# Kernel tuning notes

Hardware: AMD Instinct MI355X
Metric: run time of the kernel (lower is better)

The kernel has to match this reference:

```python
import jax, jax.numpy as jnp
import numpy as np

N_NODES = 50000   # field_size == number of graph nodes
N_EDGES = 800000  # avg degree 16
VOCAB = 200000    # feature_size
EMB = 64          # embedding_size == in_dim
HID = 64          # num_hidden
SLOPE = 0.2       # leaky relu negative slope


def setup_inputs() -> dict:
    key = jax.random.key(0)
    ks = jax.random.split(key, 20)
    s = 0.05
    d = {}
    d["features"] = jax.random.randint(ks[0], (8, N_NODES), 0, VOCAB, dtype=jnp.int32)
    d["feature_values"] = jax.random.uniform(ks[1], (8, N_NODES), dtype=jnp.float32)
    d["src"] = jax.random.randint(ks[2], (N_EDGES,), 0, N_NODES, dtype=jnp.int32)
    d["dst"] = jax.random.randint(ks[3], (N_EDGES,), 0, N_NODES, dtype=jnp.int32)
    d["emb"] = jax.random.normal(ks[4], (VOCAB, EMB), jnp.float32) * s
    # layer 0: in=64 -> heads=2, out=64 (no residual)
    d["W0"]  = jax.random.normal(ks[5], (EMB, 2 * HID), jnp.float32) * s
    d["al0"] = jax.random.normal(ks[6], (2, HID), jnp.float32) * s
    d["ar0"] = jax.random.normal(ks[7], (2, HID), jnp.float32) * s
    d["b0"]  = jnp.zeros((2 * HID,), jnp.float32)
    # layer 1: in=128 -> heads=2, out=64 (identity residual since in == heads*out)
    d["W1"]  = jax.random.normal(ks[8], (2 * HID, 2 * HID), jnp.float32) * s
    d["al1"] = jax.random.normal(ks[9], (2, HID), jnp.float32) * s
    d["ar1"] = jax.random.normal(ks[10], (2, HID), jnp.float32) * s
    d["b1"]  = jnp.zeros((2 * HID,), jnp.float32)
    # output layer: in=128 -> heads=1, out=64 (projected residual), no activation
    d["W2"]    = jax.random.normal(ks[11], (2 * HID, EMB), jnp.float32) * s
    d["al2"]   = jax.random.normal(ks[12], (1, EMB), jnp.float32) * s
    d["ar2"]   = jax.random.normal(ks[13], (1, EMB), jnp.float32) * s
    d["b2"]    = jnp.zeros((EMB,), jnp.float32)
    d["resW2"] = jax.random.normal(ks[14], (2 * HID, EMB), jnp.float32) * s
    return d


def _gat_layer(h, src, dst, W, al, ar, b, res, act):
    """DGL-style GATConv. h: [N, in], W: [in, H*D], al/ar: [H, D]."""
    N = h.shape[0]
    H, D = al.shape
    fh = (h @ W).reshape(N, H, D)                      # [N, H, D]
    el = jnp.einsum('nhd,hd->nh', fh, al)              # [N, H]
    er = jnp.einsum('nhd,hd->nh', fh, ar)              # [N, H]
    e = jax.nn.leaky_relu(el[src] + er[dst], SLOPE)    # [E, H]
    # edge softmax grouped by destination node
    m = jax.ops.segment_max(e, dst, num_segments=N)
    m = jnp.where(jnp.isfinite(m), m, 0.0)
    ex = jnp.exp(e - m[dst])
    den = jax.ops.segment_sum(ex, dst, num_segments=N)
    alpha = ex / jnp.maximum(den[dst], 1e-9)           # [E, H]
    out = jax.ops.segment_sum(alpha[:, :, None] * fh[src], dst, num_segments=N)  # [N, H, D]
    if res is not None:
        out = out + res
    out = out + b.reshape(H, D)
    if act:
        out = jax.nn.elu(out)
    return out


def reference(features, feature_values, src, dst, emb,
              W0, al0, ar0, b0, W1, al1, ar1, b1,
              W2, al2, ar2, b2, resW2):
    # embedding lookup scaled by feature values: [B, field, emb]
    fe = emb[features] * feature_values[..., None]
    h = fe[0]                                          # [N_NODES, EMB]
    # layer 0: no residual, elu, flatten heads
    h = _gat_layer(h, src, dst, W0, al0, ar0, b0, None, True).reshape(N_NODES, -1)
    # layer 1: identity residual (in == heads*out), elu, flatten heads
    res1 = h.reshape(N_NODES, 2, HID)
    h = _gat_layer(h, src, dst, W1, al1, ar1, b1, res1, True).reshape(N_NODES, -1)
    # output layer: projected residual, no activation, mean over heads
    res2 = (h @ resW2).reshape(N_NODES, 1, EMB)
    logits = _gat_layer(h, src, dst, W2, al2, ar2, b2, res2, False).mean(axis=1)
    return logits
```

## Files before the change

kernel.cpp:

```cpp
#include <hip/hip_runtime.h>


typedef __attribute__((ext_vector_type(8))) short short8;
typedef __attribute__((ext_vector_type(4))) float float4v;

__device__ __forceinline__ float lrelu(float x){ return x >= 0.f ? x : 0.2f*x; }

__device__ __forceinline__ unsigned short f2bf(float f){
  unsigned int u = __float_as_uint(f);
  u += 0x7fffu + ((u >> 16) & 1u);
  return (unsigned short)(u >> 16);
}
__device__ __forceinline__ float bf2f(unsigned short u){
  return __uint_as_float((unsigned int)u << 16);
}
__device__ __forceinline__ float rl_f(float v, int l){
  return __int_as_float(__builtin_amdgcn_readlane(__float_as_int(v), l));
}

__global__ void k_zero_i32(int* __restrict__ p, int n){
  int i = blockIdx.x*blockDim.x + threadIdx.x;
  if (i < n) p[i] = 0;
}

__global__ void k_hist(const int* __restrict__ dst, int* __restrict__ counts, int E){
  int i0 = (blockIdx.x*blockDim.x + threadIdx.x)*4;
  #pragma unroll
  for (int u = 0; u < 4; u++){
    int i = i0 + u;
    if (i < E) atomicAdd(&counts[dst[i]], 1);
  }
}

__global__ void k_scan_local(const int* __restrict__ counts, int* __restrict__ row_ptr,
                             int* __restrict__ bsum, int N){
  __shared__ int s[256];
  int t = threadIdx.x, g = blockIdx.x*256 + t;
  int v = (g < N) ? counts[g] : 0;
  s[t] = v; __syncthreads();
  #pragma unroll
  for (int off = 1; off < 256; off <<= 1){
    int x = 0;
    if (t >= off) x = s[t-off];
    __syncthreads();
    s[t] += x;
    __syncthreads();
  }
  if (g < N) row_ptr[g+1] = s[t];
  if (g == 0 && t == 0) row_ptr[0] = 0;
  if (t == 255) bsum[blockIdx.x] = s[255];
}

__global__ void k_scan_top(int* __restrict__ bsum, int nb){
  __shared__ int s[256];
  int t = threadIdx.x;
  int v = (t < nb) ? bsum[t] : 0;
  s[t] = v; __syncthreads();
  #pragma unroll
  for (int off = 1; off < 256; off <<= 1){
    int x = 0;
    if (t >= off) x = s[t-off];
    __syncthreads();
    s[t] += x;
    __syncthreads();
  }
  if (t < nb) bsum[t] = s[t] - v;
}

__global__ void k_scan_fix(int* __restrict__ row_ptr, const int* __restrict__ bsum, int N){
  int g = blockIdx.x*256 + threadIdx.x;
  if (g < N && blockIdx.x > 0) row_ptr[g+1] += bsum[blockIdx.x];
}

__global__ void k_scatter(const int* __restrict__ src, const int* __restrict__ dst,
                          const int* __restrict__ row_ptr, int* __restrict__ cursor,
                          unsigned short* __restrict__ ssrc, int E){
  int i0 = (blockIdx.x*blockDim.x + threadIdx.x)*4;
  #pragma unroll
  for (int u = 0; u < 4; u++){
    int i = i0 + u;
    if (i < E){
      int d = dst[i];
      int pos = atomicAdd(&cursor[d], 1);
      ssrc[row_ptr[d] + pos] = (unsigned short)src[i];
    }
  }
}

__global__ void k_wprep_all(const float* __restrict__ W0, const float* __restrict__ W1,
                            const float* __restrict__ W2, const float* __restrict__ rW2,
                            unsigned short* __restrict__ Wt0, unsigned short* __restrict__ Wt1,
                            unsigned short* __restrict__ Wt2){
  int id = blockIdx.x*256 + threadIdx.x;
  if (id < 128*64){
    int n = id/64, k = id%64;
    Wt0[n*64 + k] = f2bf(W0[k*128 + n]);
  } else if (id < 128*64 + 128*128){
    int j = id - 128*64; int n = j/128, k = j%128;
    Wt1[n*128 + k] = f2bf(W1[k*128 + n]);
  } else if (id < 128*64 + 2*128*128){
    int j = id - 128*64 - 128*128; int n = j/128, k = j%128;
    float v = (n < 64) ? W2[k*64 + n] : rW2[k*64 + (n - 64)];
    Wt2[n*128 + k] = f2bf(v);
  }
}

template<int IN, int H, int AMODE>
__global__ __launch_bounds__(256) void k_gemm_mfma(
    const float* __restrict__ hf,
    const int* __restrict__ feat, const float* __restrict__ fv, const float* __restrict__ emb,
    const unsigned short* __restrict__ Wt,
    const float* __restrict__ al, const float* __restrict__ ar,
    unsigned short* __restrict__ fhb,
    float* __restrict__ elr, int N){
  constexpr int KS = IN/32;
  constexpr int LDP = IN + 8;
  __shared__ unsigned short Wt_s[128*LDP];
  const int t = threadIdx.x;
  const int lane = t & 63, wid = t >> 6;
  const int l15 = lane & 15, quad = lane >> 4;
  const int row0 = blockIdx.x*64 + wid*16;

  for (int id = t; id < 128*(IN/8); id += 256){
    int r = id/(IN/8), seg = id%(IN/8);
    ((uint4*)(Wt_s + r*LDP))[seg] = ((const uint4*)(Wt + (size_t)r*IN))[seg];
  }
  short8 a[KS];
  int arow = row0 + l15;
  {
    const float* ap = nullptr;
    float sc = 1.f;
    if (AMODE == 0){
      int f = 0; sc = 0.f;
      if (arow < N){ f = feat[arow]; sc = fv[arow]; }
      ap = emb + (size_t)f*64;
    } else {
      ap = (arow < N) ? hf + (size_t)arow*IN : nullptr;
    }
    #pragma unroll
    for (int s = 0; s < KS; s++){
      short8 av = short8{0,0,0,0,0,0,0,0};
      if (ap){
        const float* p = ap + s*32 + quad*8;
        float4 v0 = ((const float4*)p)[0];
        float4 v1 = ((const float4*)p)[1];
        av[0]=(short)f2bf(v0.x*sc); av[1]=(short)f2bf(v0.y*sc);
        av[2]=(short)f2bf(v0.z*sc); av[3]=(short)f2bf(v0.w*sc);
        av[4]=(short)f2bf(v1.x*sc); av[5]=(short)f2bf(v1.y*sc);
        av[6]=(short)f2bf(v1.z*sc); av[7]=(short)f2bf(v1.w*sc);
      }
      a[s] = av;
    }
  }
  __syncthreads();

  float4v acc[8];
  #pragma unroll
  for (int nt = 0; nt < 8; nt++) acc[nt] = float4v{0.f,0.f,0.f,0.f};
  #pragma unroll
  for (int nt = 0; nt < 8; nt++){
    #pragma unroll
    for (int s = 0; s < KS; s++){
      short8 b = *(const short8*)(Wt_s + (nt*16 + l15)*LDP + s*32 + quad*8);
      acc[nt] = __builtin_amdgcn_mfma_f32_16x16x32_bf16(a[s], b, acc[nt], 0, 0, 0);
    }
  }

  float alc[8], arc[8];
  #pragma unroll
  for (int nt = 0; nt < 8; nt++){
    bool hv = (H == 2) || (nt < 4);
    alc[nt] = hv ? al[nt*16 + l15] : 0.f;
    arc[nt] = hv ? ar[nt*16 + l15] : 0.f;
  }
  #pragma unroll
  for (int reg = 0; reg < 4; reg++){
    int row = row0 + quad*4 + reg;
    bool rv = row < N;
    if (rv){
      #pragma unroll
      for (int nt = 0; nt < 8; nt++)
        fhb[(size_t)row*128 + nt*16 + l15] = f2bf(acc[nt][reg]);
    }
    float pel0 = 0.f, per0 = 0.f, pel1 = 0.f, per1 = 0.f;
    #pragma unroll
    for (int nt = 0; nt < 4; nt++){
      pel0 += acc[nt][reg]*alc[nt];     per0 += acc[nt][reg]*arc[nt];
      pel1 += acc[nt+4][reg]*alc[nt+4]; per1 += acc[nt+4][reg]*arc[nt+4];
    }
    #pragma unroll
    for (int off = 1; off < 16; off <<= 1){
      pel0 += __shfl_xor(pel0, off, 64);
      pel1 += __shfl_xor(pel1, off, 64);
      per0 += __shfl_xor(per0, off, 64);
      per1 += __shfl_xor(per1, off, 64);
    }
    if (l15 == 0 && rv){
      elr[row*4+0] = pel0;
      elr[row*4+1] = (H == 2) ? pel1 : 0.f;
      elr[row*4+2] = per0;
      elr[row*4+3] = (H == 2) ? per1 : 0.f;
    }
  }
}

template<int H>
__global__ __launch_bounds__(256) void k_agg(
    const unsigned* __restrict__ fhb, const float* __restrict__ elr,
    const int* __restrict__ row_ptr, const unsigned short* __restrict__ ssrc,
    const float* __restrict__ bias, const float* __restrict__ res,
    int act, int res_from_fh,
    float* __restrict__ out, int out_ld, int N){
  int lane = threadIdx.x & 63, wid = threadIdx.x >> 6;
  int n = blockIdx.x*4 + wid;
  if (n >= N) return;
  int beg = row_ptr[n], end = row_ptr[n+1];
  float er0 = elr[n*4+2];
  float er1 = (H == 2) ? elr[n*4+3] : 0.f;

  float x0 = 0.f, x1 = 0.f;
  {
    int i = beg + lane;
    if (i < end){
      int s = ssrc[i];
      float2 el = *(const float2*)(elr + s*4);
      x0 = __expf(fminf(lrelu(el.x + er0), 30.f));
      if (H == 2) x1 = __expf(fminf(lrelu(el.y + er1), 30.f));
    }
  }
  float d0 = x0, d1 = x1;
  for (int i = beg + lane + 64; i < end; i += 64){
    int s = ssrc[i];
    float2 el = *(const float2*)(elr + s*4);
    d0 += __expf(fminf(lrelu(el.x + er0), 30.f));
    if (H == 2) d1 += __expf(fminf(lrelu(el.y + er1), 30.f));
  }
  #pragma unroll
  for (int off = 32; off >= 1; off >>= 1){
    d0 += __shfl_xor(d0, off, 64);
    if (H == 2) d1 += __shfl_xor(d1, off, 64);
  }
  float rd0 = d0 > 0.f ? 1.f/d0 : 0.f;
  float rd1 = (H == 2 && d1 > 0.f) ? 1.f/d1 : 0.f;

  float ax = 0.f, ay = 0.f;
  for (int base = beg; base < end; base += 64){
    int i = base + lane;
    int s = 0; float a0 = 0.f, a1 = 0.f;
    if (i < end){
      s = ssrc[i];
      if (base == beg){
        a0 = x0 * rd0; if (H == 2) a1 = x1 * rd1;
      } else {
        float2 el = *(const float2*)(elr + s*4);
        a0 = __expf(fminf(lrelu(el.x + er0), 30.f)) * rd0;
        if (H == 2) a1 = __expf(fminf(lrelu(el.y + er1), 30.f)) * rd1;
      }
    }
    int cnt = min(64, end - base);
    int j0 = 0;
    if (H == 2){
      for (; j0 + 16 <= cnt; j0 += 16){
        unsigned w[16]; float aj[16];
        #pragma unroll
        for (int u = 0; u < 16; u++){
          int sj = __builtin_amdgcn_readlane(s, j0 + u);
          w[u] = fhb[(size_t)sj*64 + lane];
        }
        #pragma unroll
        for (int u = 0; u < 16; u++){
          float aj0 = rl_f(a0, j0 + u);
          float aj1 = rl_f(a1, j0 + u);
          aj[u] = (lane < 32) ? aj0 : aj1;
        }
        #pragma unroll
        for (int u = 0; u < 16; u++){
          ax += bf2f((unsigned short)(w[u] & 0xffffu)) * aj[u];
          ay += bf2f((unsigned short)(w[u] >> 16))     * aj[u];
        }
      }
      for (; j0 < cnt; j0 += 8){
        unsigned w[8]; float aj[8];
        #pragma unroll
        for (int u = 0; u < 8; u++){
          int sj = __builtin_amdgcn_readlane(s, j0 + u);
          w[u] = fhb[(size_t)sj*64 + lane];
        }
        #pragma unroll
        for (int u = 0; u < 8; u++){
          float aj0 = rl_f(a0, j0 + u);
          float aj1 = rl_f(a1, j0 + u);
          aj[u] = (lane < 32) ? aj0 : aj1;
        }
        #pragma unroll
        for (int u = 0; u < 8; u++){
          ax += bf2f((unsigned short)(w[u] & 0xffffu)) * aj[u];
          ay += bf2f((unsigned short)(w[u] >> 16))     * aj[u];
        }
      }
    } else {
      const unsigned short* fh16 = (const unsigned short*)fhb;
      for (; j0 + 16 <= cnt; j0 += 16){
        unsigned short w[16]; float aj[16];
        #pragma unroll
        for (int u = 0; u < 16; u++){
          int sj = __builtin_amdgcn_readlane(s, j0 + u);
          w[u] = fh16[(size_t)sj*128 + lane];
        }
        #pragma unroll
        for (int u = 0; u < 16; u++) aj[u] = rl_f(a0, j0 + u);
        #pragma unroll
        for (int u = 0; u < 16; u++) ax += bf2f(w[u]) * aj[u];
      }
      for (; j0 < cnt; j0 += 8){
        unsigned short w[8]; float aj[8];
        #pragma unroll
        for (int u = 0; u < 8; u++){
          int sj = __builtin_amdgcn_readlane(s, j0 + u);
          w[u] = fh16[(size_t)sj*128 + lane];
        }
        #pragma unroll
        for (int u = 0; u < 8; u++) aj[u] = rl_f(a0, j0 + u);
        #pragma unroll
        for (int u = 0; u < 8; u++) ax += bf2f(w[u]) * aj[u];
      }
    }
  }
  if (H == 2){
    int c0 = lane*2;
    float o0 = ax + bias[c0], o1 = ay + bias[c0+1];
    if (res){ o0 += res[n*128 + c0]; o1 += res[n*128 + c0+1]; }
    if (act){ o0 = o0 > 0.f ? o0 : expm1f(o0); o1 = o1 > 0.f ? o1 : expm1f(o1); }
    *(float2*)(out + n*out_ld + c0) = make_float2(o0, o1);
  } else {
    const unsigned short* fh16 = (const unsigned short*)fhb;
    float o = ax + bias[lane];
    if (res_from_fh) o += bf2f(fh16[(size_t)n*128 + 64 + lane]);
    out[n*out_ld + lane] = o;
  }
}

extern "C" void kernel_launch(void* const* d_in, const int* in_sizes, int n_in,
                              void* d_out, int out_size, void* d_ws, size_t ws_size,
                              hipStream_t stream) {
  const int*   feat = (const int*)  d_in[0];
  const float* fv   = (const float*)d_in[1];
  const int*   src  = (const int*)  d_in[2];
  const int*   dst  = (const int*)  d_in[3];
  const float* emb  = (const float*)d_in[4];
  const float* W0   = (const float*)d_in[5];
  const float* al0  = (const float*)d_in[6];
  const float* ar0  = (const float*)d_in[7];
  const float* b0   = (const float*)d_in[8];
  const float* W1   = (const float*)d_in[9];
  const float* al1  = (const float*)d_in[10];
  const float* ar1  = (const float*)d_in[11];
  const float* b1   = (const float*)d_in[12];
  const float* W2   = (const float*)d_in[13];
  const float* al2  = (const float*)d_in[14];
  const float* ar2  = (const float*)d_in[15];
  const float* b2   = (const float*)d_in[16];
  const float* rW2  = (const float*)d_in[17];
  const int N = in_sizes[0] / 8;
  const int E = in_sizes[2];

  size_t off = 0;
  auto alloc = [&](size_t bytes) -> void* {
    void* p = (char*)d_ws + off;
    off = (off + bytes + 255) & ~(size_t)255;
    return p;
  };
  unsigned short* P1 = (unsigned short*)alloc((size_t)N*128*sizeof(unsigned short));
  float* P2     = (float*)alloc((size_t)N*128*sizeof(float));
  float* P3     = (float*)alloc((size_t)N*128*sizeof(float));
  float* elr    = (float*)alloc((size_t)N*4*sizeof(float));
  int* row_ptr  = (int*)alloc((size_t)(N+1)*sizeof(int));
  int* counts   = (int*)alloc((size_t)2*N*sizeof(int));
  int* cursor   = counts + N;
  unsigned short* ssrc = (unsigned short*)alloc((size_t)E*sizeof(unsigned short));
  int* bsum     = (int*)alloc(256*sizeof(int));
  unsigned short* Wt0 = (unsigned short*)alloc((size_t)128*64*sizeof(unsigned short));
  unsigned short* Wt1 = (unsigned short*)alloc((size_t)128*128*sizeof(unsigned short));
  unsigned short* Wt2 = (unsigned short*)alloc((size_t)128*128*sizeof(unsigned short));

  int nb1 = (N + 255) / 256;
  k_zero_i32<<<(2*N + 255)/256, 256, 0, stream>>>(counts, 2*N);
  k_hist<<<(E/4 + 255)/256, 256, 0, stream>>>(dst, counts, E);
  k_scan_local<<<nb1, 256, 0, stream>>>(counts, row_ptr, bsum, N);
  k_scan_top<<<1, 256, 0, stream>>>(bsum, nb1);
  k_scan_fix<<<nb1, 256, 0, stream>>>(row_ptr, bsum, N);
  k_scatter<<<(E/4 + 255)/256, 256, 0, stream>>>(src, dst, row_ptr, cursor, ssrc, E);
  k_wprep_all<<<(128*64 + 2*128*128 + 255)/256, 256, 0, stream>>>(
      W0, W1, W2, rW2, Wt0, Wt1, Wt2);

  int gt = (N + 63)/64;
  int nagg = (N + 3)/4;
  k_gemm_mfma<64,2,0><<<gt, 256, 0, stream>>>(nullptr, feat, fv, emb,
      Wt0, al0, ar0, P1, elr, N);
  k_agg<2><<<nagg, 256, 0, stream>>>((unsigned*)P1, elr, row_ptr, ssrc, b0, nullptr,
                                     1, 0, P2, 128, N);
  k_gemm_mfma<128,2,1><<<gt, 256, 0, stream>>>(P2, nullptr, nullptr, nullptr,
      Wt1, al1, ar1, P1, elr, N);
  k_agg<2><<<nagg, 256, 0, stream>>>((unsigned*)P1, elr, row_ptr, ssrc, b1, P2,
                                     1, 0, P3, 128, N);
  k_gemm_mfma<128,1,1><<<gt, 256, 0, stream>>>(P3, nullptr, nullptr, nullptr,
      Wt2, al2, ar2, P1, elr, N);
  k_agg<1><<<nagg, 256, 0, stream>>>((unsigned*)P1, elr, row_ptr, ssrc, b2, nullptr,
                                     0, 1, (float*)d_out, 64, N);
}
```

Before: 374.3 us.

## Split wavefront into two half-waves gathering two neighbor rows with wider loads

The aggregation kernel now has each half of the 64-lane wavefront process a different neighbor. Each lane loads 8 bytes (uint2) of the bf16 feature row instead of 4, or 4 bytes instead of 2 in the single-head case, and accumulates four partial sums. A final cross-half shuffle combines the halves, and only 32 lanes write wider float4/float2 outputs. The aim is to halve the number of serialized gather instructions per neighbor and widen memory transactions, at the cost of an extra shuffle reduction and idle lanes in the epilogue. The zero-fill kernel is also replaced by hipMemsetAsync.

```diff
diff --git a/kernel.cpp b/kernel.cpp
--- a/kernel.cpp
+++ b/kernel.cpp
@@ -16,11 +16,6 @@
 }
 __device__ __forceinline__ float rl_f(float v, int l){
   return __int_as_float(__builtin_amdgcn_readlane(__float_as_int(v), l));
-}
-
-__global__ void k_zero_i32(int* __restrict__ p, int n){
-  int i = blockIdx.x*blockDim.x + threadIdx.x;
-  if (i < n) p[i] = 0;
 }
 
 __global__ void k_hist(const int* __restrict__ dst, int* __restrict__ counts, int E){
@@ -243,7 +238,11 @@
   float rd0 = d0 > 0.f ? 1.f/d0 : 0.f;
   float rd1 = (H == 2 && d1 > 0.f) ? 1.f/d1 : 0.f;
 
-  float ax = 0.f, ay = 0.f;
+  const int hl = lane & 31;
+  const bool loA = lane < 32;
+  const bool hi16 = (lane & 16) != 0;
+
+  float ac0 = 0.f, ac1 = 0.f, ac2 = 0.f, ac3 = 0.f;
   for (int base = beg; base < end; base += 64){
     int i = base + lane;
     int s = 0; float a0 = 0.f, a1 = 0.f;
@@ -261,82 +260,126 @@
     int j0 = 0;
     if (H == 2){
       for (; j0 + 16 <= cnt; j0 += 16){
-        unsigned w[16]; float aj[16];
-        #pragma unroll
-        for (int u = 0; u < 16; u++){
-          int sj = __builtin_amdgcn_readlane(s, j0 + u);
-          w[u] = fhb[(size_t)sj*64 + lane];
-        }
-        #pragma unroll
-        for (int u = 0; u < 16; u++){
-          float aj0 = rl_f(a0, j0 + u);
-          float aj1 = rl_f(a1, j0 + u);
-          aj[u] = (lane < 32) ? aj0 : aj1;
-        }
-        #pragma unroll
-        for (int u = 0; u < 16; u++){
-          ax += bf2f((unsigned short)(w[u] & 0xffffu)) * aj[u];
-          ay += bf2f((unsigned short)(w[u] >> 16))     * aj[u];
+        uint2 w[8]; float aj[8];
+        #pragma unroll
+        for (int p = 0; p < 8; p++){
+          int sA = __builtin_amdgcn_readlane(s, j0 + 2*p);
+          int sB = __builtin_amdgcn_readlane(s, j0 + 2*p + 1);
+          int r = loA ? sA : sB;
+          w[p] = *(const uint2*)(fhb + (size_t)r*64 + hl*2);
+        }
+        #pragma unroll
+        for (int p = 0; p < 8; p++){
+          float a0A = rl_f(a0, j0 + 2*p),   a1A = rl_f(a1, j0 + 2*p);
+          float a0B = rl_f(a0, j0 + 2*p+1), a1B = rl_f(a1, j0 + 2*p+1);
+          float a0s = loA ? a0A : a0B, a1s = loA ? a1A : a1B;
+          aj[p] = hi16 ? a1s : a0s;
+        }
+        #pragma unroll
+        for (int p = 0; p < 8; p++){
+          ac0 += bf2f((unsigned short)(w[p].x & 0xffffu)) * aj[p];
+          ac1 += bf2f((unsigned short)(w[p].x >> 16))     * aj[p];
+          ac2 += bf2f((unsigned short)(w[p].y & 0xffffu)) * aj[p];
+          ac3 += bf2f((unsigned short)(w[p].y >> 16))     * aj[p];
         }
       }
       for (; j0 < cnt; j0 += 8){
+        uint2 w[4]; float aj[4];
+        #pragma unroll
+        for (int p = 0; p < 4; p++){
+          int sA = __builtin_amdgcn_readlane(s, j0 + 2*p);
+          int sB = __builtin_amdgcn_readlane(s, j0 + 2*p + 1);
+          int r = loA ? sA : sB;
+          w[p] = *(const uint2*)(fhb + (size_t)r*64 + hl*2);
+        }
+        #pragma unroll
+        for (int p = 0; p < 4; p++){
+          float a0A = rl_f(a0, j0 + 2*p),   a1A = rl_f(a1, j0 + 2*p);
+          float a0B = rl_f(a0, j0 + 2*p+1), a1B = rl_f(a1, j0 + 2*p+1);
+          float a0s = loA ? a0A : a0B, a1s = loA ? a1A : a1B;
+          aj[p] = hi16 ? a1s : a0s;
+        }
+        #pragma unroll
+        for (int p = 0; p < 4; p++){
+          ac0 += bf2f((unsigned short)(w[p].x & 0xffffu)) * aj[p];
+          ac1 += bf2f((unsigned short)(w[p].x >> 16))     * aj[p];
+          ac2 += bf2f((unsigned short)(w[p].y & 0xffffu)) * aj[p];
+          ac3 += bf2f((unsigned short)(w[p].y >> 16))     * aj[p];
+        }
+      }
+    } else {
+      for (; j0 + 16 <= cnt; j0 += 16){
         unsigned w[8]; float aj[8];
         #pragma unroll
-        for (int u = 0; u < 8; u++){
-          int sj = __builtin_amdgcn_readlane(s, j0 + u);
-          w[u] = fhb[(size_t)sj*64 + lane];
-        }
-        #pragma unroll
-        for (int u = 0; u < 8; u++){
-          float aj0 = rl_f(a0, j0 + u);
-          float aj1 = rl_f(a1, j0 + u);
-          aj[u] = (lane < 32) ? aj0 : aj1;
-        }
-        #pragma unroll
-        for (int u = 0; u < 8; u++){
-          ax += bf2f((unsigned short)(w[u] & 0xffffu)) * aj[u];
-          ay += bf2f((unsigned short)(w[u] >> 16))     * aj[u];
-        }
-      }
-    } else {
-      const unsigned short* fh16 = (const unsigned short*)fhb;
-      for (; j0 + 16 <= cnt; j0 += 16){
-        unsigned short w[16]; float aj[16];
-        #pragma unroll
-        for (int u = 0; u < 16; u++){
-          int sj = __builtin_amdgcn_readlane(s, j0 + u);
-          w[u] = fh16[(size_t)sj*128 + lane];
-        }
-        #pragma unroll
-        for (int u = 0; u < 16; u++) aj[u] = rl_f(a0, j0 + u);
-        #pragma unroll
-        for (int u = 0; u < 16; u++) ax += bf2f(w[u]) * aj[u];
+        for (int p = 0; p < 8; p++){
+          int sA = __builtin_amdgcn_readlane(s, j0 + 2*p);
+          int sB = __builtin_amdgcn_readlane(s, j0 + 2*p + 1);
+          int r = loA ? sA : sB;
+          w[p] = fhb[(size_t)r*64 + hl];
+        }
+        #pragma unroll
+        for (int p = 0; p < 8; p++){
+          float aA = rl_f(a0, j0 + 2*p), aB = rl_f(a0, j0 + 2*p+1);
+          aj[p] = loA ? aA : aB;
+        }
+        #pragma unroll
+        for (int p = 0; p < 8; p++){
+          ac0 += bf2f((unsigned short)(w[p] & 0xffffu)) * aj[p];
+          ac1 += bf2f((unsigned short)(w[p] >> 16))     * aj[p];
+        }
       }
       for (; j0 < cnt; j0 += 8){
-        unsigned short w[8]; float aj[8];
-        #pragma unroll
-        for (int u = 0; u < 8; u++){
-          int sj = __builtin_amdgcn_readlane(s, j0 + u);
-          w[u] = fh16[(size_t)sj*128 + lane];
-        }
-        #pragma unroll
-        for (int u = 0; u < 8; u++) aj[u] = rl_f(a0, j0 + u);
-        #pragma unroll
-        for (int u = 0; u < 8; u++) ax += bf2f(w[u]) * aj[u];
-      }
-    }
-  }
+        unsigned w[4]; float aj[4];
+        #pragma unroll
+        for (int p = 0; p < 4; p++){
+          int sA = __builtin_amdgcn_readlane(s, j0 + 2*p);
+          int sB = __builtin_amdgcn_readlane(s, j0 + 2*p + 1);
+          int r = loA ? sA : sB;
+          w[p] = fhb[(size_t)r*64 + hl];
+        }
+        #pragma unroll
+        for (int p = 0; p < 4; p++){
+          float aA = rl_f(a0, j0 + 2*p), aB = rl_f(a0, j0 + 2*p+1);
+          aj[p] = loA ? aA : aB;
+        }
+        #pragma unroll
+        for (int p = 0; p < 4; p++){
+          ac0 += bf2f((unsigned short)(w[p] & 0xffffu)) * aj[p];
+          ac1 += bf2f((unsigned short)(w[p] >> 16))     * aj[p];
+        }
+      }
+    }
+  }
+  ac0 += __shfl_xor(ac0, 32, 64);
+  ac1 += __shfl_xor(ac1, 32, 64);
+  if (H == 2){ ac2 += __shfl_xor(ac2, 32, 64); ac3 += __shfl_xor(ac3, 32, 64); }
+
   if (H == 2){
-    int c0 = lane*2;
-    float o0 = ax + bias[c0], o1 = ay + bias[c0+1];
-    if (res){ o0 += res[n*128 + c0]; o1 += res[n*128 + c0+1]; }
-    if (act){ o0 = o0 > 0.f ? o0 : expm1f(o0); o1 = o1 > 0.f ? o1 : expm1f(o1); }
-    *(float2*)(out + n*out_ld + c0) = make_float2(o0, o1);
+    if (lane < 32){
+      int c0 = hl*4;
+      float4 b4 = *(const float4*)(bias + c0);
+      float o0 = ac0 + b4.x, o1 = ac1 + b4.y, o2 = ac2 + b4.z, o3 = ac3 + b4.w;
+      if (res){
+        float4 r4 = *(const float4*)(res + (size_t)n*128 + c0);
+        o0 += r4.x; o1 += r4.y; o2 += r4.z; o3 += r4.w;
+      }
+      if (act){
+        o0 = o0 > 0.f ? o0 : expm1f(o0); o1 = o1 > 0.f ? o1 : expm1f(o1);
+        o2 = o2 > 0.f ? o2 : expm1f(o2); o3 = o3 > 0.f ? o3 : expm1f(o3);
+      }
+      *(float4*)(out + (size_t)n*out_ld + c0) = make_float4(o0, o1, o2, o3);
+    }
   } else {
-    const unsigned short* fh16 = (const unsigned short*)fhb;
-    float o = ax + bias[lane];
-    if (res_from_fh) o += bf2f(fh16[(size_t)n*128 + 64 + lane]);
-    out[n*out_ld + lane] = o;
+    if (lane < 32){
+      int c0 = hl*2;
+      float o0 = ac0 + bias[c0], o1 = ac1 + bias[c0+1];
+      if (res_from_fh){
+        unsigned rw = fhb[(size_t)n*64 + 32 + hl];
+        o0 += bf2f((unsigned short)(rw & 0xffffu));
+        o1 += bf2f((unsigned short)(rw >> 16));
+      }
+      *(float2*)(out + (size_t)n*out_ld + c0) = make_float2(o0, o1);
+    }
   }
 }
 
@@ -384,7 +427,7 @@
   unsigned short* Wt2 = (unsigned short*)alloc((size_t)128*128*sizeof(unsigned short));
 
   int nb1 = (N + 255) / 256;
-  k_zero_i32<<<(2*N + 255)/256, 256, 0, stream>>>(counts, 2*N);
+  hipMemsetAsync(counts, 0, (size_t)2*N*sizeof(int), stream);
   k_hist<<<(E/4 + 255)/256, 256, 0, stream>>>(dst, counts, E);
   k_scan_local<<<nb1, 256, 0, stream>>>(counts, row_ptr, bsum, N);
   k_scan_top<<<1, 256, 0, stream>>>(bsum, nb1);
```

After: 382.5 us. 2.2% more time.

## Fuse all stages into one persistent cooperative kernel with grid syncs

Applied to the files above, without the earlier changes.

Replaces the twelve separate launches (CSR build, weight prep, three GEMM plus aggregation layer pairs) with one cooperative persistent kernel. Phases are separated by grid.sync and use grid-stride loops, and the old multi-launch path is kept as a fallback. The goal is to remove per-launch overhead and tail gaps between small kernels. The fused GEMM phase reads weights straight from global memory instead of staging them in LDS. Each grid-wide barrier costs time, and the grid is capped at 4 blocks per CU, which may limit latency hiding in the gather-bound aggregation.

```diff
diff --git a/kernel.cpp b/kernel.cpp
--- a/kernel.cpp
+++ b/kernel.cpp
@@ -1,5 +1,8 @@
 #include <hip/hip_runtime.h>
-
+#include <hip/hip_cooperative_groups.h>
+
+
+namespace cg = cooperative_groups;
 
 typedef __attribute__((ext_vector_type(8))) short short8;
 typedef __attribute__((ext_vector_type(4))) float float4v;
@@ -18,326 +21,407 @@
   return __int_as_float(__builtin_amdgcn_readlane(__float_as_int(v), l));
 }
 
-__global__ void k_zero_i32(int* __restrict__ p, int n){
-  int i = blockIdx.x*blockDim.x + threadIdx.x;
-  if (i < n) p[i] = 0;
-}
-
-__global__ void k_hist(const int* __restrict__ dst, int* __restrict__ counts, int E){
-  int i0 = (blockIdx.x*blockDim.x + threadIdx.x)*4;
+
+__device__ void wprep_body(const float* W0, const float* W1, const float* W2,
+                           const float* rW2, unsigned short* Wt0,
+                           unsigned short* Wt1, unsigned short* Wt2,
+                           int gtid, int gsz){
+  for (int id = gtid; id < 128*64 + 2*128*128; id += gsz){
+    if (id < 128*64){
+      int n = id/64, k = id%64;
+      Wt0[n*64 + k] = f2bf(W0[k*128 + n]);
+    } else if (id < 128*64 + 128*128){
+      int j = id - 128*64; int n = j/128, k = j%128;
+      Wt1[n*128 + k] = f2bf(W1[k*128 + n]);
+    } else {
+      int j = id - 128*64 - 128*128; int n = j/128, k = j%128;
+      float v = (n < 64) ? W2[k*64 + n] : rW2[k*64 + (n - 64)];
+      Wt2[n*128 + k] = f2bf(v);
+    }
+  }
+}
+
+__device__ void hist_body(const int* dst, int* counts, int E, int gtid, int gsz){
+  for (int base = gtid*4; base < E; base += gsz*4){
+    #pragma unroll
+    for (int u = 0; u < 4; u++){
+      int i = base + u;
+      if (i < E) atomicAdd(&counts[dst[i]], 1);
+    }
+  }
+}
+
+__device__ void scatter_body(const int* src, const int* dst, const int* row_ptr,
+                             int* cursor, unsigned short* ssrc, int E,
+                             int gtid, int gsz){
+  for (int base = gtid*4; base < E; base += gsz*4){
+    #pragma unroll
+    for (int u = 0; u < 4; u++){
+      int i = base + u;
+      if (i < E){
+        int d = dst[i];
+        int pos = atomicAdd(&cursor[d], 1);
+        ssrc[row_ptr[d] + pos] = (unsigned short)src[i];
+      }
+    }
+  }
+}
+
+template<int IN, int H, int AMODE>
+__device__ void gemm_phase(
+    const float* __restrict__ hf,
+    const int* __restrict__ feat, const float* __restrict__ fv, const float* __restrict__ emb,
+    const unsigned short* __restrict__ Wt,
+    const float* __restrict__ al, const float* __restrict__ ar,
+    unsigned short* __restrict__ fhb, float* __restrict__ elr,
+    int N, int bid, int nb, int t){
+  constexpr int KS = IN/32;
+  const int lane = t & 63, wid = t >> 6;
+  const int l15 = lane & 15, quad = lane >> 4;
+
+  float alc[8], arc[8];
   #pragma unroll
-  for (int u = 0; u < 4; u++){
-    int i = i0 + u;
-    if (i < E) atomicAdd(&counts[dst[i]], 1);
-  }
-}
-
-__global__ void k_scan_local(const int* __restrict__ counts, int* __restrict__ row_ptr,
-                             int* __restrict__ bsum, int N){
+  for (int nt = 0; nt < 8; nt++){
+    bool hv = (H == 2) || (nt < 4);
+    alc[nt] = hv ? al[nt*16 + l15] : 0.f;
+    arc[nt] = hv ? ar[nt*16 + l15] : 0.f;
+  }
+
+  const int ntiles = (N + 63)/64;
+  for (int tile = bid; tile < ntiles; tile += nb){
+    const int row0 = tile*64 + wid*16;
+    short8 a[KS];
+    int arow = row0 + l15;
+    {
+      const float* ap = nullptr;
+      float sc = 1.f;
+      if (AMODE == 0){
+        int f = 0; sc = 0.f;
+        if (arow < N){ f = feat[arow]; sc = fv[arow]; }
+        ap = emb + (size_t)f*64;
+      } else {
+        ap = (arow < N) ? hf + (size_t)arow*IN : nullptr;
+      }
+      #pragma unroll
+      for (int s = 0; s < KS; s++){
+        short8 av = short8{0,0,0,0,0,0,0,0};
+        if (ap){
+          const float* p = ap + s*32 + quad*8;
+          float4 v0 = ((const float4*)p)[0];
+          float4 v1 = ((const float4*)p)[1];
+          av[0]=(short)f2bf(v0.x*sc); av[1]=(short)f2bf(v0.y*sc);
+          av[2]=(short)f2bf(v0.z*sc); av[3]=(short)f2bf(v0.w*sc);
+          av[4]=(short)f2bf(v1.x*sc); av[5]=(short)f2bf(v1.y*sc);
+          av[6]=(short)f2bf(v1.z*sc); av[7]=(short)f2bf(v1.w*sc);
+        }
+        a[s] = av;
+      }
+    }
+    float4v acc[8];
+    #pragma unroll
+    for (int nt = 0; nt < 8; nt++) acc[nt] = float4v{0.f,0.f,0.f,0.f};
+    #pragma unroll
+    for (int nt = 0; nt < 8; nt++){
+      #pragma unroll
+      for (int s = 0; s < KS; s++){
+        short8 b = *(const short8*)(Wt + (size_t)(nt*16 + l15)*IN + s*32 + quad*8);
+        acc[nt] = __builtin_amdgcn_mfma_f32_16x16x32_bf16(a[s], b, acc[nt], 0, 0, 0);
+      }
+    }
+    #pragma unroll
+    for (int reg = 0; reg < 4; reg++){
+      int row = row0 + quad*4 + reg;
+      bool rv = row < N;
+      if (rv){
+        #pragma unroll
+        for (int nt = 0; nt < 8; nt++)
+          fhb[(size_t)row*128 + nt*16 + l15] = f2bf(acc[nt][reg]);
+      }
+      float pel0 = 0.f, per0 = 0.f, pel1 = 0.f, per1 = 0.f;
+      #pragma unroll
+      for (int nt = 0; nt < 4; nt++){
+        pel0 += acc[nt][reg]*alc[nt];     per0 += acc[nt][reg]*arc[nt];
+        pel1 += acc[nt+4][reg]*alc[nt+4]; per1 += acc[nt+4][reg]*arc[nt+4];
+      }
+      #pragma unroll
+      for (int off = 1; off < 16; off <<= 1){
+        pel0 += __shfl_xor(pel0, off, 64);
+        pel1 += __shfl_xor(pel1, off, 64);
+        per0 += __shfl_xor(per0, off, 64);
+        per1 += __shfl_xor(per1, off, 64);
+      }
+      if (l15 == 0 && rv){
+        elr[row*4+0] = pel0;
+        elr[row*4+1] = (H == 2) ? pel1 : 0.f;
+        elr[row*4+2] = per0;
+        elr[row*4+3] = (H == 2) ? per1 : 0.f;
+      }
+    }
+  }
+}
+
+template<int H>
+__device__ void agg_phase(
+    const unsigned* __restrict__ fhb, const float* __restrict__ elr,
+    const int* __restrict__ row_ptr, const unsigned short* __restrict__ ssrc,
+    const float* __restrict__ bias, const float* __restrict__ res,
+    int act, int res_from_fh,
+    float* __restrict__ out, int out_ld, int N, int bid, int nb, int t){
+  const int lane = t & 63, wid = t >> 6;
+  for (int n = bid*4 + wid; n < N; n += nb*4){
+    int beg = row_ptr[n], end = row_ptr[n+1];
+    float er0 = elr[n*4+2];
+    float er1 = (H == 2) ? elr[n*4+3] : 0.f;
+
+    float x0 = 0.f, x1 = 0.f;
+    {
+      int i = beg + lane;
+      if (i < end){
+        int s = ssrc[i];
+        float2 el = *(const float2*)(elr + s*4);
+        x0 = __expf(fminf(lrelu(el.x + er0), 30.f));
+        if (H == 2) x1 = __expf(fminf(lrelu(el.y + er1), 30.f));
+      }
+    }
+    float d0 = x0, d1 = x1;
+    for (int i = beg + lane + 64; i < end; i += 64){
+      int s = ssrc[i];
+      float2 el = *(const float2*)(elr + s*4);
+      d0 += __expf(fminf(lrelu(el.x + er0), 30.f));
+      if (H == 2) d1 += __expf(fminf(lrelu(el.y + er1), 30.f));
+    }
+    #pragma unroll
+    for (int off = 32; off >= 1; off >>= 1){
+      d0 += __shfl_xor(d0, off, 64);
+      if (H == 2) d1 += __shfl_xor(d1, off, 64);
+    }
+    float rd0 = d0 > 0.f ? 1.f/d0 : 0.f;
+    float rd1 = (H == 2 && d1 > 0.f) ? 1.f/d1 : 0.f;
+
+    float ax = 0.f, ay = 0.f;
+    for (int base = beg; base < end; base += 64){
+      int i = base + lane;
+      int s = 0; float a0 = 0.f, a1 = 0.f;
+      if (i < end){
+        s = ssrc[i];
+        if (base == beg){
+          a0 = x0 * rd0; if (H == 2) a1 = x1 * rd1;
+        } else {
+          float2 el = *(const float2*)(elr + s*4);
+          a0 = __expf(fminf(lrelu(el.x + er0), 30.f)) * rd0;
+          if (H == 2) a1 = __expf(fminf(lrelu(el.y + er1), 30.f)) * rd1;
+        }
+      }
+      int cnt = min(64, end - base);
+      int j0 = 0;
+      if (H == 2){
+        for (; j0 + 16 <= cnt; j0 += 16){
+          unsigned w[16]; float aj[16];
+          #pragma unroll
+          for (int u = 0; u < 16; u++){
+            int sj = __builtin_amdgcn_readlane(s, j0 + u);
+            w[u] = fhb[(size_t)sj*64 + lane];
+          }
+          #pragma unroll
+          for (int u = 0; u < 16; u++){
+            float aj0 = rl_f(a0, j0 + u);
+            float aj1 = rl_f(a1, j0 + u);
+            aj[u] = (lane < 32) ? aj0 : aj1;
+          }
+          #pragma unroll
+          for (int u = 0; u < 16; u++){
+            ax += bf2f((unsigned short)(w[u] & 0xffffu)) * aj[u];
+            ay += bf2f((unsigned short)(w[u] >> 16))     * aj[u];
+          }
+        }
+        for (; j0 < cnt; j0 += 8){
+          unsigned w[8]; float aj[8];
+          #pragma unroll
+          for (int u = 0; u < 8; u++){
+            int sj = __builtin_amdgcn_readlane(s, j0 + u);
+            w[u] = fhb[(size_t)sj*64 + lane];
+          }
+          #pragma unroll
+          for (int u = 0; u < 8; u++){
+            float aj0 = rl_f(a0, j0 + u);
+            float aj1 = rl_f(a1, j0 + u);
+            aj[u] = (lane < 32) ? aj0 : aj1;
+          }
+          #pragma unroll
+          for (int u = 0; u < 8; u++){
+            ax += bf2f((unsigned short)(w[u] & 0xffffu)) * aj[u];
+            ay += bf2f((unsigned short)(w[u] >> 16))     * aj[u];
+          }
+        }
+      } else {
+        const unsigned short* fh16 = (const unsigned short*)fhb;
+        for (; j0 + 16 <= cnt; j0 += 16){
+          unsigned short w[16]; float aj[16];
+          #pragma unroll
+          for (int u = 0; u < 16; u++){
+            int sj = __builtin_amdgcn_readlane(s, j0 + u);
+            w[u] = fh16[(size_t)sj*128 + lane];
+          }
+          #pragma unroll
+          for (int u = 0; u < 16; u++) aj[u] = rl_f(a0, j0 + u);
+          #pragma unroll
+          for (int u = 0; u < 16; u++) ax += bf2f(w[u]) * aj[u];
+        }
+        for (; j0 < cnt; j0 += 8){
+          unsigned short w[8]; float aj[8];
+          #pragma unroll
+          for (int u = 0; u < 8; u++){
+            int sj = __builtin_amdgcn_readlane(s, j0 + u);
+            w[u] = fh16[(size_t)sj*128 + lane];
+          }
+          #pragma unroll
+          for (int u = 0; u < 8; u++) aj[u] = rl_f(a0, j0 + u);
+          #pragma unroll
+          for (int u = 0; u < 8; u++) ax += bf2f(w[u]) * aj[u];
+        }
+      }
+    }
+    if (H == 2){
+      int c0 = lane*2;
+      float o0 = ax + bias[c0], o1 = ay + bias[c0+1];
+      if (res){ o0 += res[(size_t)n*128 + c0]; o1 += res[(size_t)n*128 + c0+1]; }
+      if (act){ o0 = o0 > 0.f ? o0 : expm1f(o0); o1 = o1 > 0.f ? o1 : expm1f(o1); }
+      *(float2*)(out + (size_t)n*out_ld + c0) = make_float2(o0, o1);
+    } else {
+      const unsigned short* fh16 = (const unsigned short*)fhb;
+      float o = ax + bias[lane];
+      if (res_from_fh) o += bf2f(fh16[(size_t)n*128 + 64 + lane]);
+      out[(size_t)n*out_ld + lane] = o;
+    }
+  }
+}
+
+
+__global__ __launch_bounds__(256, 4) void k_mega(
+    const int* feat, const float* fv, const int* src, const int* dst,
+    const float* emb,
+    const float* W0, const float* al0, const float* ar0, const float* b0,
+    const float* W1, const float* al1, const float* ar1, const float* b1,
+    const float* W2, const float* al2, const float* ar2, const float* b2,
+    const float* rW2,
+    unsigned short* P1, float* P2, float* P3, float* elr,
+    int* row_ptr, int* counts, int* cursor, unsigned short* ssrc, int* bsum,
+    unsigned short* Wt0, unsigned short* Wt1, unsigned short* Wt2,
+    float* out, int N, int E){
+  __shared__ int si[256];
+  cg::grid_group grid = cg::this_grid();
+  const int t = threadIdx.x, bid = blockIdx.x, nb = gridDim.x;
+  const int gtid = bid*256 + t, gsz = nb*256;
+
+  for (int id = gtid; id < 2*N; id += gsz) counts[id] = 0;
+  wprep_body(W0, W1, W2, rW2, Wt0, Wt1, Wt2, gtid, gsz);
+  __threadfence(); grid.sync();
+
+  hist_body(dst, counts, E, gtid, gsz);
+  __threadfence(); grid.sync();
+
+  const int SB = (N + 255)/256;
+  if (bid < SB){
+    int v = (gtid < N) ? counts[gtid] : 0;
+    si[t] = v; __syncthreads();
+    #pragma unroll
+    for (int off = 1; off < 256; off <<= 1){
+      int x = (t >= off) ? si[t-off] : 0;
+      __syncthreads(); si[t] += x; __syncthreads();
+    }
+    if (gtid < N) row_ptr[gtid+1] = si[t];
+    if (gtid == 0) row_ptr[0] = 0;
+    if (t == 255) bsum[bid] = si[255];
+  }
+  __threadfence(); grid.sync();
+  if (bid == 0){
+    int v = (t < SB) ? bsum[t] : 0;
+    si[t] = v; __syncthreads();
+    #pragma unroll
+    for (int off = 1; off < 256; off <<= 1){
+      int x = (t >= off) ? si[t-off] : 0;
+      __syncthreads(); si[t] += x; __syncthreads();
+    }
+    if (t < SB) bsum[t] = si[t] - v;
+  }
+  __threadfence(); grid.sync();
+  if (bid > 0 && bid < SB && gtid < N) row_ptr[gtid+1] += bsum[bid];
+  __threadfence(); grid.sync();
+
+  scatter_body(src, dst, row_ptr, cursor, ssrc, E, gtid, gsz);
+  __threadfence(); grid.sync();
+
+  gemm_phase<64,2,0>(nullptr, feat, fv, emb, Wt0, al0, ar0, P1, elr, N, bid, nb, t);
+  __threadfence(); grid.sync();
+  agg_phase<2>((unsigned*)P1, elr, row_ptr, ssrc, b0, nullptr, 1, 0, P2, 128, N, bid, nb, t);
+  __threadfence(); grid.sync();
+  gemm_phase<128,2,1>(P2, nullptr, nullptr, nullptr, Wt1, al1, ar1, P1, elr, N, bid, nb, t);
+  __threadfence(); grid.sync();
+  agg_phase<2>((unsigned*)P1, elr, row_ptr, ssrc, b1, P2, 1, 0, P3, 128, N, bid, nb, t);
+  __threadfence(); grid.sync();
+  gemm_phase<128,1,1>(P3, nullptr, nullptr, nullptr, Wt2, al2, ar2, P1, elr, N, bid, nb, t);
+  __threadfence(); grid.sync();
+  agg_phase<1>((unsigned*)P1, elr, row_ptr, ssrc, b2, nullptr, 0, 1, out, 64, N, bid, nb, t);
+}
+
+
+__global__ __launch_bounds__(256) void k_hist(const int* dst, int* counts, int E){
+  hist_body(dst, counts, E, blockIdx.x*256 + threadIdx.x, gridDim.x*256);
+}
+__global__ __launch_bounds__(256) void k_scatter(const int* src, const int* dst,
+    const int* row_ptr, int* cursor, unsigned short* ssrc, int E){
+  scatter_body(src, dst, row_ptr, cursor, ssrc, E, blockIdx.x*256 + threadIdx.x, gridDim.x*256);
+}
+__global__ __launch_bounds__(256) void k_wprep(const float* W0, const float* W1,
+    const float* W2, const float* rW2,
+    unsigned short* Wt0, unsigned short* Wt1, unsigned short* Wt2){
+  wprep_body(W0, W1, W2, rW2, Wt0, Wt1, Wt2, blockIdx.x*256 + threadIdx.x, gridDim.x*256);
+}
+__global__ void k_scan_local(const int* counts, int* row_ptr, int* bsum, int N){
   __shared__ int s[256];
   int t = threadIdx.x, g = blockIdx.x*256 + t;
   int v = (g < N) ? counts[g] : 0;
   s[t] = v; __syncthreads();
   #pragma unroll
   for (int off = 1; off < 256; off <<= 1){
-    int x = 0;
-    if (t >= off) x = s[t-off];
-    __syncthreads();
-    s[t] += x;
-    __syncthreads();
+    int x = (t >= off) ? s[t-off] : 0;
+    __syncthreads(); s[t] += x; __syncthreads();
   }
   if (g < N) row_ptr[g+1] = s[t];
   if (g == 0 && t == 0) row_ptr[0] = 0;
   if (t == 255) bsum[blockIdx.x] = s[255];
 }
-
-__global__ void k_scan_top(int* __restrict__ bsum, int nb){
+__global__ void k_scan_top(int* bsum, int nb){
   __shared__ int s[256];
   int t = threadIdx.x;
   int v = (t < nb) ? bsum[t] : 0;
   s[t] = v; __syncthreads();
   #pragma unroll
   for (int off = 1; off < 256; off <<= 1){
-    int x = 0;
-    if (t >= off) x = s[t-off];
-    __syncthreads();
-    s[t] += x;
-    __syncthreads();
+    int x = (t >= off) ? s[t-off] : 0;
+    __syncthreads(); s[t] += x; __syncthreads();
   }
   if (t < nb) bsum[t] = s[t] - v;
 }
-
-__global__ void k_scan_fix(int* __restrict__ row_ptr, const int* __restrict__ bsum, int N){
+__global__ void k_scan_fix(int* row_ptr, const int* bsum, int N){
   int g = blockIdx.x*256 + threadIdx.x;
   if (g < N && blockIdx.x > 0) row_ptr[g+1] += bsum[blockIdx.x];
 }
-
-__global__ void k_scatter(const int* __restrict__ src, const int* __restrict__ dst,
-                          const int* __restrict__ row_ptr, int* __restrict__ cursor,
-                          unsigned short* __restrict__ ssrc, int E){
-  int i0 = (blockIdx.x*blockDim.x + threadIdx.x)*4;
-  #pragma unroll
-  for (int u = 0; u < 4; u++){
-    int i = i0 + u;
-    if (i < E){
-      int d = dst[i];
-      int pos = atomicAdd(&cursor[d], 1);
-      ssrc[row_ptr[d] + pos] = (unsigned short)src[i];
-    }
-  }
-}
-
-__global__ void k_wprep_all(const float* __restrict__ W0, const float* __restrict__ W1,
-                            const float* __restrict__ W2, const float* __restrict__ rW2,
-                            unsigned short* __restrict__ Wt0, unsigned short* __restrict__ Wt1,
-                            unsigned short* __restrict__ Wt2){
-  int id = blockIdx.x*256 + threadIdx.x;
-  if (id < 128*64){
-    int n = id/64, k = id%64;
-    Wt0[n*64 + k] = f2bf(W0[k*128 + n]);
-  } else if (id < 128*64 + 128*128){
-    int j = id - 128*64; int n = j/128, k = j%128;
-    Wt1[n*128 + k] = f2bf(W1[k*128 + n]);
-  } else if (id < 128*64 + 2*128*128){
-    int j = id - 128*64 - 128*128; int n = j/128, k = j%128;
-    float v = (n < 64) ? W2[k*64 + n] : rW2[k*64 + (n - 64)];
-    Wt2[n*128 + k] = f2bf(v);
-  }
-}
-
 template<int IN, int H, int AMODE>
-__global__ __launch_bounds__(256) void k_gemm_mfma(
-    const float* __restrict__ hf,
-    const int* __restrict__ feat, const float* __restrict__ fv, const float* __restrict__ emb,
-    const unsigned short* __restrict__ Wt,
-    const float* __restrict__ al, const float* __restrict__ ar,
-    unsigned short* __restrict__ fhb,
-    float* __restrict__ elr, int N){
-  constexpr int KS = IN/32;
-  constexpr int LDP = IN + 8;
-  __shared__ unsigned short Wt_s[128*LDP];
-  const int t = threadIdx.x;
-  const int lane = t & 63, wid = t >> 6;
-  const int l15 = lane & 15, quad = lane >> 4;
-  const int row0 = blockIdx.x*64 + wid*16;
-
-  for (int id = t; id < 128*(IN/8); id += 256){
-    int r = id/(IN/8), seg = id%(IN/8);
-    ((uint4*)(Wt_s + r*LDP))[seg] = ((const uint4*)(Wt + (size_t)r*IN))[seg];
-  }
-  short8 a[KS];
-  int arow = row0 + l15;
-  {
-    const float* ap = nullptr;
-    float sc = 1.f;
-    if (AMODE == 0){
-      int f = 0; sc = 0.f;
-      if (arow < N){ f = feat[arow]; sc = fv[arow]; }
-      ap = emb + (size_t)f*64;
-    } else {
-      ap = (arow < N) ? hf + (size_t)arow*IN : nullptr;
-    }
-    #pragma unroll
-    for (int s = 0; s < KS; s++){
-      short8 av = short8{0,0,0,0,0,0,0,0};
-      if (ap){
-        const float* p = ap + s*32 + quad*8;
-        float4 v0 = ((const float4*)p)[0];
-        float4 v1 = ((const float4*)p)[1];
-        av[0]=(short)f2bf(v0.x*sc); av[1]=(short)f2bf(v0.y*sc);
-        av[2]=(short)f2bf(v0.z*sc); av[3]=(short)f2bf(v0.w*sc);
-        av[4]=(short)f2bf(v1.x*sc); av[5]=(short)f2bf(v1.y*sc);
-        av[6]=(short)f2bf(v1.z*sc); av[7]=(short)f2bf(v1.w*sc);
-      }
-      a[s] = av;
-    }
-  }
-  __syncthreads();
-
-  float4v acc[8];
-  #pragma unroll
-  for (int nt = 0; nt < 8; nt++) acc[nt] = float4v{0.f,0.f,0.f,0.f};
-  #pragma unroll
-  for (int nt = 0; nt < 8; nt++){
-    #pragma unroll
-    for (int s = 0; s < KS; s++){
-      short8 b = *(const short8*)(Wt_s + (nt*16 + l15)*LDP + s*32 + quad*8);
-      acc[nt] = __builtin_amdgcn_mfma_f32_16x16x32_bf16(a[s], b, acc[nt], 0, 0, 0);
-    }
-  }
-
-  float alc[8], arc[8];
-  #pragma unroll
-  for (int nt = 0; nt < 8; nt++){
-    bool hv = (H == 2) || (nt < 4);
-    alc[nt] = hv ? al[nt*16 + l15] : 0.f;
-    arc[nt] = hv ? ar[nt*16 + l15] : 0.f;
-  }
-  #pragma unroll
-  for (int reg = 0; reg < 4; reg++){
-    int row = row0 + quad*4 + reg;
-    bool rv = row < N;
-    if (rv){
-      #pragma unroll
-      for (int nt = 0; nt < 8; nt++)
-        fhb[(size_t)row*128 + nt*16 + l15] = f2bf(acc[nt][reg]);
-    }
-    float pel0 = 0.f, per0 = 0.f, pel1 = 0.f, per1 = 0.f;
-    #pragma unroll
-    for (int nt = 0; nt < 4; nt++){
-      pel0 += acc[nt][reg]*alc[nt];     per0 += acc[nt][reg]*arc[nt];
-      pel1 += acc[nt+4][reg]*alc[nt+4]; per1 += acc[nt+4][reg]*arc[nt+4];
-    }
-    #pragma unroll
-    for (int off = 1; off < 16; off <<= 1){
-      pel0 += __shfl_xor(pel0, off, 64);
-      pel1 += __shfl_xor(pel1, off, 64);
-      per0 += __shfl_xor(per0, off, 64);
-      per1 += __shfl_xor(per1, off, 64);
-    }
-    if (l15 == 0 && rv){
-      elr[row*4+0] = pel0;
-      elr[row*4+1] = (H == 2) ? pel1 : 0.f;
-      elr[row*4+2] = per0;
-      elr[row*4+3] = (H == 2) ? per1 : 0.f;
-    }
-  }
-}
-
+__global__ __launch_bounds__(256) void k_gemm(
+    const float* hf, const int* feat, const float* fv, const float* emb,
+    const unsigned short* Wt, const float* al, const float* ar,
+    unsigned short* fhb, float* elr, int N){
+  gemm_phase<IN,H,AMODE>(hf, feat, fv, emb, Wt, al, ar, fhb, elr, N,
+                         blockIdx.x, gridDim.x, threadIdx.x);
+}
 template<int H>
 __global__ __launch_bounds__(256) void k_agg(
-    const unsigned* __restrict__ fhb, const float* __restrict__ elr,
-    const int* __restrict__ row_ptr, const unsigned short* __restrict__ ssrc,
-    const float* __restrict__ bias, const float* __restrict__ res,
-    int act, int res_from_fh,
-    float* __restrict__ out, int out_ld, int N){
-  int lane = threadIdx.x & 63, wid = threadIdx.x >> 6;
-  int n = blockIdx.x*4 + wid;
-  if (n >= N) return;
-  int beg = row_ptr[n], end = row_ptr[n+1];
-  float er0 = elr[n*4+2];
-  float er1 = (H == 2) ? elr[n*4+3] : 0.f;
-
-  float x0 = 0.f, x1 = 0.f;
-  {
-    int i = beg + lane;
-    if (i < end){
-      int s = ssrc[i];
-      float2 el = *(const float2*)(elr + s*4);
-      x0 = __expf(fminf(lrelu(el.x + er0), 30.f));
-      if (H == 2) x1 = __expf(fminf(lrelu(el.y + er1), 30.f));
-    }
-  }
-  float d0 = x0, d1 = x1;
-  for (int i = beg + lane + 64; i < end; i += 64){
-    int s = ssrc[i];
-    float2 el = *(const float2*)(elr + s*4);
-    d0 += __expf(fminf(lrelu(el.x + er0), 30.f));
-    if (H == 2) d1 += __expf(fminf(lrelu(el.y + er1), 30.f));
-  }
-  #pragma unroll
-  for (int off = 32; off >= 1; off >>= 1){
-    d0 += __shfl_xor(d0, off, 64);
-    if (H == 2) d1 += __shfl_xor(d1, off, 64);
-  }
-  float rd0 = d0 > 0.f ? 1.f/d0 : 0.f;
-  float rd1 = (H == 2 && d1 > 0.f) ? 1.f/d1 : 0.f;
-
-  float ax = 0.f, ay = 0.f;
-  for (int base = beg; base < end; base += 64){
-    int i = base + lane;
-    int s = 0; float a0 = 0.f, a1 = 0.f;
-    if (i < end){
-      s = ssrc[i];
-      if (base == beg){
-        a0 = x0 * rd0; if (H == 2) a1 = x1 * rd1;
-      } else {
-        float2 el = *(const float2*)(elr + s*4);
-        a0 = __expf(fminf(lrelu(el.x + er0), 30.f)) * rd0;
-        if (H == 2) a1 = __expf(fminf(lrelu(el.y + er1), 30.f)) * rd1;
-      }
-    }
-    int cnt = min(64, end - base);
-    int j0 = 0;
-    if (H == 2){
-      for (; j0 + 16 <= cnt; j0 += 16){
-        unsigned w[16]; float aj[16];
-        #pragma unroll
-        for (int u = 0; u < 16; u++){
-          int sj = __builtin_amdgcn_readlane(s, j0 + u);
-          w[u] = fhb[(size_t)sj*64 + lane];
-        }
-        #pragma unroll
-        for (int u = 0; u < 16; u++){
-          float aj0 = rl_f(a0, j0 + u);
-          float aj1 = rl_f(a1, j0 + u);
-          aj[u] = (lane < 32) ? aj0 : aj1;
-        }
-        #pragma unroll
-        for (int u = 0; u < 16; u++){
-          ax += bf2f((unsigned short)(w[u] & 0xffffu)) * aj[u];
-          ay += bf2f((unsigned short)(w[u] >> 16))     * aj[u];
-        }
-      }
-      for (; j0 < cnt; j0 += 8){
-        unsigned w[8]; float aj[8];
-        #pragma unroll
-        for (int u = 0; u < 8; u++){
-          int sj = __builtin_amdgcn_readlane(s, j0 + u);
-          w[u] = fhb[(size_t)sj*64 + lane];
-        }
-        #pragma unroll
-        for (int u = 0; u < 8; u++){
-          float aj0 = rl_f(a0, j0 + u);
-          float aj1 = rl_f(a1, j0 + u);
-          aj[u] = (lane < 32) ? aj0 : aj1;
-        }
-        #pragma unroll
-        for (int u = 0; u < 8; u++){
-          ax += bf2f((unsigned short)(w[u] & 0xffffu)) * aj[u];
-          ay += bf2f((unsigned short)(w[u] >> 16))     * aj[u];
-        }
-      }
-    } else {
-      const unsigned short* fh16 = (const unsigned short*)fhb;
-      for (; j0 + 16 <= cnt; j0 += 16){
-        unsigned short w[16]; float aj[16];
-        #pragma unroll
-        for (int u = 0; u < 16; u++){
-          int sj = __builtin_amdgcn_readlane(s, j0 + u);
-          w[u] = fh16[(size_t)sj*128 + lane];
-        }
-        #pragma unroll
-        for (int u = 0; u < 16; u++) aj[u] = rl_f(a0, j0 + u);
-        #pragma unroll
-        for (int u = 0; u < 16; u++) ax += bf2f(w[u]) * aj[u];
-      }
-      for (; j0 < cnt; j0 += 8){
-        unsigned short w[8]; float aj[8];
-        #pragma unroll
-        for (int u = 0; u < 8; u++){
-          int sj = __builtin_amdgcn_readlane(s, j0 + u);
-          w[u] = fh16[(size_t)sj*128 + lane];
-        }
-        #pragma unroll
-        for (int u = 0; u < 8; u++) aj[u] = rl_f(a0, j0 + u);
-        #pragma unroll
-        for (int u = 0; u < 8; u++) ax += bf2f(w[u]) * aj[u];
-      }
-    }
-  }
-  if (H == 2){
-    int c0 = lane*2;
-    float o0 = ax + bias[c0], o1 = ay + bias[c0+1];
-    if (res){ o0 += res[n*128 + c0]; o1 += res[n*128 + c0+1]; }
-    if (act){ o0 = o0 > 0.f ? o0 : expm1f(o0); o1 = o1 > 0.f ? o1 : expm1f(o1); }
-    *(float2*)(out + n*out_ld + c0) = make_float2(o0, o1);
-  } else {
-    const unsigned short* fh16 = (const unsigned short*)fhb;
-    float o = ax + bias[lane];
-    if (res_from_fh) o += bf2f(fh16[(size_t)n*128 + 64 + lane]);
-    out[n*out_ld + lane] = o;
-  }
+    const unsigned* fhb, const float* elr, const int* row_ptr,
+    const unsigned short* ssrc, const float* bias, const float* res,
+    int act, int res_from_fh, float* out, int out_ld, int N){
+  agg_phase<H>(fhb, elr, row_ptr, ssrc, bias, res, act, res_from_fh,
+               out, out_ld, N, blockIdx.x, gridDim.x, threadIdx.x);
 }
 
 extern "C" void kernel_launch(void* const* d_in, const int* in_sizes, int n_in,
@@ -361,8 +445,8 @@
   const float* ar2  = (const float*)d_in[15];
   const float* b2   = (const float*)d_in[16];
   const float* rW2  = (const float*)d_in[17];
-  const int N = in_sizes[0] / 8;
-  const int E = in_sizes[2];
+  int N = in_sizes[0] / 8;
+  int E = in_sizes[2];
 
   size_t off = 0;
   auto alloc = [&](size_t bytes) -> void* {
@@ -382,29 +466,49 @@
   unsigned short* Wt0 = (unsigned short*)alloc((size_t)128*64*sizeof(unsigned short));
   unsigned short* Wt1 = (unsigned short*)alloc((size_t)128*128*sizeof(unsigned short));
   unsigned short* Wt2 = (unsigned short*)alloc((size_t)128*128*sizeof(unsigned short));
+  float* out = (float*)d_out;
+
+  void* args[] = {
+    &feat, &fv, &src, &dst, &emb,
+    &W0, &al0, &ar0, &b0,
+    &W1, &al1, &ar1, &b1,
+    &W2, &al2, &ar2, &b2, &rW2,
+    &P1, &P2, &P3, &elr,
+    &row_ptr, &counts, &cursor, &ssrc, &bsum,
+    &Wt0, &Wt1, &Wt2,
+    &out, &N, &E
+  };
+  bool coop = false;
+  int bpcu = 0;
+  if (hipOccupancyMaxActiveBlocksPerMultiprocessor(&bpcu, (const void*)k_mega, 256, 0)
+        == hipSuccess && bpcu >= 2){
+    if (bpcu > 4) bpcu = 4;
+    int grid = bpcu * 256;
+    if (hipLaunchCooperativeKernel((void*)k_mega, dim3(grid), dim3(256),
+                                   args, 0, stream) == hipSuccess)
+      coop = true;
+  }
+  if (coop) return;
 
   int nb1 = (N + 255) / 256;
-  k_zero_i32<<<(2*N + 255)/256, 256, 0, stream>>>(counts, 2*N);
+  hipMemsetAsync(counts, 0, (size_t)2*N*sizeof(int), stream);
   k_hist<<<(E/4 + 255)/256, 256, 0, stream>>>(dst, counts, E);
   k_scan_local<<<nb1, 256, 0, stream>>>(counts, row_ptr, bsum, N);
   k_scan_top<<<1, 256, 0, stream>>>(bsum, nb1);
   k_scan_fix<<<nb1, 256, 0, stream>>>(row_ptr, bsum, N);
   k_scatter<<<(E/4 + 255)/256, 256, 0, stream>>>(src, dst, row_ptr, cursor, ssrc, E);
-  k_wprep_all<<<(128*64 + 2*128*128 + 255)/256, 256, 0, stream>>>(
+  k_wprep<<<(128*64 + 2*128*128 + 255)/256, 256, 0, stream>>>(
       W0, W1, W2, rW2, Wt0, Wt1, Wt2);
 
   int gt = (N + 63)/64;
   int nagg = (N + 3)/4;
-  k_gemm_mfma<64,2,0><<<gt, 256, 0, stream>>>(nullptr, feat, fv, emb,
-      Wt0, al0, ar0, P1, elr, N);
+  k_gemm<64,2,0><<<gt, 256, 0, stream>>>(nullptr, feat, fv, emb, Wt0, al0, ar0, P1, elr, N);
   k_agg<2><<<nagg, 256, 0, stream>>>((unsigned*)P1, elr, row_ptr, ssrc, b0, nullptr,
                                      1, 0, P2, 128, N);
-  k_gemm_mfma<128,2,1><<<gt, 256, 0, stream>>>(P2, nullptr, nullptr, nullptr,
-      Wt1, al1, ar1, P1, elr, N);
+  k_gemm<128,2,1><<<gt, 256, 0, stream>>>(P2, nullptr, nullptr, nullptr, Wt1, al1, ar1, P1, elr, N);
   k_agg<2><<<nagg, 256, 0, stream>>>((unsigned*)P1, elr, row_ptr, ssrc, b1, P2,
                                      1, 0, P3, 128, N);
-  k_gemm_mfma<128,1,1><<<gt, 256, 0, stream>>>(P3, nullptr, nullptr, nullptr,
-      Wt2, al2, ar2, P1, elr, N);
+  k_gemm<128,1,1><<<gt, 256, 0, stream>>>(P3, nullptr, nullptr, nullptr, Wt2, al2, ar2, P1, elr, N);
   k_agg<1><<<nagg, 256, 0, stream>>>((unsigned*)P1, elr, row_ptr, ssrc, b2, nullptr,
                                      0, 1, (float*)d_out, 64, N);
 }
```

Result: slower. 528.1 us (+41.1%).
